# Kernel tuning notes

Measured on AMD Instinct MI355X. Metric: run time of the kernel, lower is better.

The kernel has to match this reference:

```python
import jax, jax.numpy as jnp
import numpy as np
from jax import lax

BN_EPS = 1e-5


def setup_inputs() -> dict:
    key = jax.random.key(0)
    ks = jax.random.split(key, 12)
    h, c, i, kk = 8, 64, 96, 3
    c2, n, d = c // 2, 8, 512
    std = lambda f: np.float32(f)
    return {
        "X": jax.random.normal(ks[0], (h, n, d), jnp.float32),
        "lin_w": jax.random.normal(ks[1], (h, c2, d), jnp.float32) * std(d ** -0.5),
        "lin_b": jax.random.normal(ks[2], (h, c2), jnp.float32) * std(0.02),
        "bn_gamma": jnp.ones((h, c2), jnp.float32),
        "bn_beta": jnp.zeros((h, c2), jnp.float32),
        "px": jax.random.normal(ks[3], (1, 1, c2, 1, i), jnp.float32) * std(c ** -0.5),
        "py": jax.random.normal(ks[4], (1, 1, c2, i, 1), jnp.float32) * std(c ** -0.5),
        "kw": jax.random.normal(ks[5], (h, c, c), jnp.float32) * std(c ** -0.5),
        "kb": jax.random.normal(ks[6], (h, c), jnp.float32) * std(0.02),
        "vw": jax.random.normal(ks[7], (h, c, c), jnp.float32) * std(c ** -0.5),
        "vb": jax.random.normal(ks[8], (h, c), jnp.float32) * std(0.02),
        "sw": jax.random.normal(ks[9], (c, c, kk, kk), jnp.float32) * std((c * kk * kk) ** -0.5),
        "sb": jax.random.normal(ks[10], (c,), jnp.float32) * std(0.02),
    }


def reference(X, lin_w, lin_b, bn_gamma, bn_beta, px, py, kw, kb, vw, vb, sw, sb):
    h, n, _ = X.shape
    c = kw.shape[1]
    c2 = c // 2
    i = px.shape[-1]
    kk = sw.shape[-1]

    # --- MultiheadEmbedding: per-head Linear -> BatchNorm1d(train) -> ReLU ---
    y = jnp.einsum('hnd,hcd->hnc', X, lin_w) + lin_b[:, None, :]      # (h, n, c2)
    mu = y.mean(axis=1, keepdims=True)
    var = y.var(axis=1, keepdims=True)                                 # biased, as BN
    y = (y - mu) * lax.rsqrt(var + BN_EPS) * bn_gamma[:, None, :] + bn_beta[:, None, :]
    y = jax.nn.relu(y)
    M = jnp.transpose(y, (1, 0, 2))[..., None, None]                   # (n, h, c2, 1, 1)

    # --- PositionalEncoding: concat x/y translated copies -> (n, h, c, i, i) ---
    P = jnp.concatenate([
        jnp.broadcast_to(M + px, (n, h, c2, i, i)),
        jnp.broadcast_to(M + py, (n, h, c2, i, i)),
    ], axis=2)                                                          # (n, h, c, i, i)

    # --- TransposeAttention ---
    # grouped 1x1 key conv (groups = h)
    kp = jnp.einsum('nhcij,hdc->nhdij', P, kw) + kb[None, :, :, None, None]
    # score conv over each (c, i, i) map, shared across heads, scaled
    x = kp.reshape(n * h, c, i, i)
    s = lax.conv_general_dilated(x, sw, (1, 1), 'SAME',
                                 dimension_numbers=('NCHW', 'OIHW', 'NCHW'))
    s = (s + sb[None, :, None, None]) / np.float32((c * kk * kk) ** 0.5)
    w = jax.nn.softmax(s.reshape(n, h, c, i, i), axis=1)                # softmax over heads
    # grouped 1x1 value conv, weighted sum over heads
    vp = jnp.einsum('nhcij,hdc->nhdij', P, vw) + vb[None, :, :, None, None]
    T = (w * vp).sum(axis=1)                                            # (n, c, i, i)
    return (T, M, P, w)
```

## Files before the change

kernel.cpp:

```cpp
#include <hip/hip_runtime.h>
#include <math.h>

#define H    8
#define N    8
#define D    512
#define C    64
#define C2   32
#define I    96
#define II   9216

#define OFF_T 0
#define OFF_M 4718592
#define OFF_P 4720640
#define OFF_W 42469376

#define WS_AK 0
#define WS_AV 4096
#define WS_BK 8192
#define WS_BV 57344
#define WS_CK 106496
#define WS_CV 155648
#define WS_SS 204800
#define WS_SP 241664
#define WS_SQ 278528
#define WS_F  315392
#define WS_G2 352256
#define WS_H2 499712

__device__ __forceinline__ int bcls(int x) { return x == 0 ? 0 : (x == I - 1 ? 2 : 1); }

__global__ __launch_bounds__(256) void irf_embed(
    const float* __restrict__ X, const float* __restrict__ lin_w,
    const float* __restrict__ lin_b, const float* __restrict__ gamma,
    const float* __restrict__ beta, float* __restrict__ out)
{
    const int h = blockIdx.x, t = threadIdx.x;
    const int n = t >> 5, cc = t & 31;

    __shared__ float Xs[N * D];
    __shared__ float ys[N * C2];
    __shared__ float scale_s[C2], shift_s[C2];

    const float4* Xg  = (const float4*)(X + (size_t)h * N * D);
    float4*       Xs4 = (float4*)Xs;
    for (int idx = t; idx < N * D / 4; idx += 256) Xs4[idx] = Xg[idx];
    __syncthreads();

    const float4* wrow = (const float4*)(lin_w + ((size_t)h * C2 + cc) * D);
    const float4* xrow = (const float4*)(Xs + n * D);
    float a0 = 0.f, a1 = 0.f, a2 = 0.f, a3 = 0.f;
    #pragma unroll 4
    for (int k = 0; k < D / 4; ++k) {
        float4 xv = xrow[k], wv = wrow[k];
        a0 = fmaf(xv.x, wv.x, a0); a1 = fmaf(xv.y, wv.y, a1);
        a2 = fmaf(xv.z, wv.z, a2); a3 = fmaf(xv.w, wv.w, a3);
    }
    float y = (a0 + a1) + (a2 + a3) + lin_b[h * C2 + cc];
    ys[n * C2 + cc] = y;
    __syncthreads();

    if (t < C2) {
        float s = 0.f, ss = 0.f;
        #pragma unroll
        for (int j = 0; j < N; ++j) { float v = ys[j * C2 + t]; s += v; ss += v * v; }
        float mu  = s * (1.0f / N);
        float var = ss * (1.0f / N) - mu * mu;
        float sc  = rsqrtf(var + 1e-5f) * gamma[h * C2 + t];
        scale_s[t] = sc;
        shift_s[t] = beta[h * C2 + t] - mu * sc;
    }
    __syncthreads();

    float v = fmaxf(fmaf(y, scale_s[cc], shift_s[cc]), 0.0f);
    out[OFF_M + (n * H + h) * C2 + cc] = v;
}

__global__ __launch_bounds__(256) void irf_factors_a(
    const float* __restrict__ kw, const float* __restrict__ kb,
    const float* __restrict__ vw, const float* __restrict__ vb,
    const float* __restrict__ px, const float* __restrict__ py,
    const float* __restrict__ sw, const float* __restrict__ out,
    float* __restrict__ ws)
{
    int gid = blockIdx.x * 256 + threadIdx.x;
    if (gid < 4096) {
        int id = gid, d = id & 63, h = (id >> 6) & 7, n = id >> 9;
        const float* kwr = kw + ((size_t)h * C + d) * C;
        const float* vwr = vw + ((size_t)h * C + d) * C;
        const float* Mr  = out + OFF_M + (n * H + h) * C2;
        float ak = kb[h * C + d], av = vb[h * C + d];
        #pragma unroll 8
        for (int c = 0; c < C2; ++c) {
            float m = Mr[c];
            ak = fmaf(kwr[c] + kwr[C2 + c], m, ak);
            av = fmaf(vwr[c] + vwr[C2 + c], m, av);
        }
        ws[WS_AK + id] = ak;
        ws[WS_AV + id] = av;
    } else if (gid < 4096 + 49152) {
        int id = gid - 4096, d = id & 63, r = id >> 6, b = r % I, h = r / I;
        const float* kwr = kw + ((size_t)h * C + d) * C;
        const float* vwr = vw + ((size_t)h * C + d) * C;
        float bk = 0.f, bv = 0.f, ck = 0.f, cv = 0.f;
        #pragma unroll 8
        for (int c = 0; c < C2; ++c) {
            float pxv = px[c * I + b], pyv = py[c * I + b];
            bk = fmaf(kwr[c], pxv, bk);       bv = fmaf(vwr[c], pxv, bv);
            ck = fmaf(kwr[C2 + c], pyv, ck);  cv = fmaf(vwr[C2 + c], pyv, cv);
        }
        ws[WS_BK + id] = bk;
        ws[WS_BV + (h * C + d) * I + b] = bv;
        ws[WS_CK + id] = ck; ws[WS_CV + id] = cv;
    } else if (gid < 4096 + 49152 + 4096) {
        int id = gid - (4096 + 49152), d = id & 63, e = id >> 6;
        float k9[3][3];
        const float* swr = sw + (size_t)(e * C + d) * 9;
        #pragma unroll
        for (int p = 0; p < 3; ++p)
            #pragma unroll
            for (int q = 0; q < 3; ++q) k9[p][q] = swr[p * 3 + q];
        #pragma unroll
        for (int ra = 0; ra < 3; ++ra) {
            int pmin = (ra == 0) ? 1 : 0, pmax = (ra == 2) ? 1 : 2;
            #pragma unroll
            for (int q = 0; q < 3; ++q) {
                float sp = 0.f;
                for (int p = pmin; p <= pmax; ++p) sp += k9[p][q];
                ws[WS_SP + ((ra * 3 + q) * C + e) * C + d] = sp;
            }
            #pragma unroll
            for (int rb = 0; rb < 3; ++rb) {
                int qmin = (rb == 0) ? 1 : 0, qmax = (rb == 2) ? 1 : 2;
                float ssv = 0.f;
                for (int p = pmin; p <= pmax; ++p)
                    for (int q = qmin; q <= qmax; ++q) ssv += k9[p][q];
                ws[WS_SS + ((ra * 3 + rb) * C + e) * C + d] = ssv;
            }
        }
        #pragma unroll
        for (int rb = 0; rb < 3; ++rb) {
            int qmin = (rb == 0) ? 1 : 0, qmax = (rb == 2) ? 1 : 2;
            #pragma unroll
            for (int p = 0; p < 3; ++p) {
                float sq = 0.f;
                for (int q = qmin; q <= qmax; ++q) sq += k9[p][q];
                ws[WS_SQ + ((rb * 3 + p) * C + e) * C + d] = sq;
            }
        }
    }
}

__global__ __launch_bounds__(256) void irf_factors_b(float* __restrict__ ws)
{
    int gid = blockIdx.x * 256 + threadIdx.x;
    if (gid < 36864) {
        int id = gid, e = id & 63, h = (id >> 6) & 7, cls = (id >> 9) % 9, n = id / 4608;
        const float* ak = ws + WS_AK + (n * H + h) * C;
        const float* ss = ws + WS_SS + (cls * C + e) * C;
        float acc = 0.f;
        #pragma unroll 8
        for (int d = 0; d < C; ++d) acc = fmaf(ak[d], ss[d], acc);
        ws[WS_F + id] = acc;
    } else if (gid < 36864 + 147456) {
        int j = gid - 36864, b = j % I, e = (j / I) & 63, h = (j / (I * C)) & 7, ra = j / (I * C * H);
        int rb = bcls(b), qmin = (rb == 0) ? 1 : 0, qmax = (rb == 2) ? 1 : 2;
        float acc = 0.f;
        for (int q = qmin; q <= qmax; ++q) {
            const float* sp = ws + WS_SP + ((ra * 3 + q) * C + e) * C;
            const float* bk = ws + WS_BK + ((h * I) + (b + q - 1)) * C;
            #pragma unroll 8
            for (int d = 0; d < C; ++d) acc = fmaf(sp[d], bk[d], acc);
        }
        ws[WS_G2 + j] = acc;
    } else if (gid < 36864 + 2 * 147456) {
        int j = gid - 36864 - 147456, e = j & 63, h = (j >> 6) & 7, rb = (j >> 9) % 3, a = j / 1536;
        int ra = bcls(a), pmin = (ra == 0) ? 1 : 0, pmax = (ra == 2) ? 1 : 2;
        float acc = 0.f;
        for (int p = pmin; p <= pmax; ++p) {
            const float* sq = ws + WS_SQ + ((rb * 3 + p) * C + e) * C;
            const float* ck = ws + WS_CK + ((h * I) + (a + p - 1)) * C;
            #pragma unroll 8
            for (int d = 0; d < C; ++d) acc = fmaf(sq[d], ck[d], acc);
        }
        ws[WS_H2 + j] = acc;
    }
}

__global__ __launch_bounds__(256) void irf_site(
    const float* __restrict__ px, const float* __restrict__ py,
    const float* __restrict__ sb, const float* __restrict__ ws,
    float* __restrict__ out)
{
    const int bid = blockIdx.x;
    const int n = bid / I, a = bid - n * I;
    const int ra = bcls(a);
    const int t = threadIdx.x;

    __shared__ float FH[3 * 512];
    __shared__ float AC[512];
    __shared__ float Ms_[256];
    __shared__ float pxs[C2 * I];
    __shared__ float pys[C2];

    {
        const float* fsrc = ws + WS_F + (n * 9 + ra * 3) * 512;
        const float* hsrc = ws + WS_H2 + a * 1536;
        for (int o = t; o < 1536; o += 256) FH[o] = fsrc[o] + hsrc[o] + sb[o & 63];
        const float* avsrc = ws + WS_AV + n * 512;
        for (int o = t; o < 512; o += 256) {
            int h = o >> 6, e = o & 63;
            AC[o] = avsrc[o] + ws[WS_CV + ((h * I) + a) * C + e];
        }
        Ms_[t] = out[OFF_M + n * 256 + t];
        for (int o = t; o < C2 * I; o += 256) pxs[o] = px[o];
        if (t < C2) pys[t] = py[t * I + a];
    }
    __syncthreads();

    const float inv24 = 1.0f / 24.0f;

    #pragma unroll
    for (int it = 0; it < 6; ++it) {
        int idx = it * 256 + t;
        int e = idx / 24, b4 = idx - e * 24;
        int b = b4 * 4;

        float4 sv[H];
        float4 mx = make_float4(-1e30f, -1e30f, -1e30f, -1e30f);
        #pragma unroll
        for (int h = 0; h < H; ++h) {
            float4 g2 = ((const float4*)(ws + WS_G2 + ((ra * H + h) * C + e) * I))[b4];
            float fh1 = FH[512 + h * 64 + e];
            float fx = fh1, fw = fh1;
            if (b4 == 0)  fx = FH[h * 64 + e];
            if (b4 == 23) fw = FH[1024 + h * 64 + e];
            float4 s;
            s.x = (fx  + g2.x) * inv24;
            s.y = (fh1 + g2.y) * inv24;
            s.z = (fh1 + g2.z) * inv24;
            s.w = (fw  + g2.w) * inv24;
            sv[h] = s;
            mx.x = fmaxf(mx.x, s.x); mx.y = fmaxf(mx.y, s.y);
            mx.z = fmaxf(mx.z, s.z); mx.w = fmaxf(mx.w, s.w);
        }
        float4 sum = make_float4(0.f, 0.f, 0.f, 0.f);
        #pragma unroll
        for (int h = 0; h < H; ++h) {
            sv[h].x = __expf(sv[h].x - mx.x); sum.x += sv[h].x;
            sv[h].y = __expf(sv[h].y - mx.y); sum.y += sv[h].y;
            sv[h].z = __expf(sv[h].z - mx.z); sum.z += sv[h].z;
            sv[h].w = __expf(sv[h].w - mx.w); sum.w += sv[h].w;
        }
        float4 rs;
        rs.x = 1.0f / sum.x; rs.y = 1.0f / sum.y;
        rs.z = 1.0f / sum.z; rs.w = 1.0f / sum.w;

        float4 T = make_float4(0.f, 0.f, 0.f, 0.f);
        #pragma unroll
        for (int h = 0; h < H; ++h) {
            float4 w;
            w.x = sv[h].x * rs.x; w.y = sv[h].y * rs.y;
            w.z = sv[h].z * rs.z; w.w = sv[h].w * rs.w;
            ((float4*)(out + OFF_W + (size_t)(((n * H + h) * C + e) * I + a) * I))[b4] = w;
            float ac = AC[h * 64 + e];
            float4 bv = ((const float4*)(ws + WS_BV + (h * C + e) * I))[b4];
            T.x = fmaf(w.x, ac + bv.x, T.x);
            T.y = fmaf(w.y, ac + bv.y, T.y);
            T.z = fmaf(w.z, ac + bv.z, T.z);
            T.w = fmaf(w.w, ac + bv.w, T.w);
        }
        ((float4*)(out + OFF_T + (size_t)((n * C + e) * I + a) * I))[b4] = T;
    }

    #pragma unroll
    for (int it = 0; it < 48; ++it) {
        int idx = it * 256 + t;
        int b4 = idx % 24, rem = idx / 24;
        int c = rem & 63, h = rem >> 6;
        float4 v;
        if (c < C2) {
            float base = Ms_[h * C2 + c];
            float4 p4 = ((const float4*)(pxs + c * I))[b4];
            v.x = base + p4.x; v.y = base + p4.y;
            v.z = base + p4.z; v.w = base + p4.w;
        } else {
            float bb = Ms_[h * C2 + c - C2] + pys[c - C2];
            v = make_float4(bb, bb, bb, bb);
        }
        ((float4*)(out + OFF_P + (size_t)(((n * H + h) * C + c) * I + a) * I))[b4] = v;
    }
}

extern "C" void kernel_launch(void* const* d_in, const int* in_sizes, int n_in,
                              void* d_out, int out_size, void* d_ws, size_t ws_size,
                              hipStream_t stream) {
    const float* X     = (const float*)d_in[0];
    const float* lin_w = (const float*)d_in[1];
    const float* lin_b = (const float*)d_in[2];
    const float* gamma = (const float*)d_in[3];
    const float* beta  = (const float*)d_in[4];
    const float* px    = (const float*)d_in[5];
    const float* py    = (const float*)d_in[6];
    const float* kw    = (const float*)d_in[7];
    const float* kb    = (const float*)d_in[8];
    const float* vw    = (const float*)d_in[9];
    const float* vb    = (const float*)d_in[10];
    const float* sw    = (const float*)d_in[11];
    const float* sb    = (const float*)d_in[12];

    float* out = (float*)d_out;
    float* ws  = (float*)d_ws;

    irf_embed    <<<8,    256, 0, stream>>>(X, lin_w, lin_b, gamma, beta, out);
    irf_factors_a<<<224,  256, 0, stream>>>(kw, kb, vw, vb, px, py, sw, out, ws);
    irf_factors_b<<<1296, 256, 0, stream>>>(ws);
    irf_site     <<<768,  256, 0, stream>>>(px, py, sb, ws, out);
}
```

Before: 411.6 us.

## Restructure site kernel into per-plane softmax and P-write kernels with transposed factors

Splits the per-(n,a) site kernel into a softmax kernel organized per (n,e) plane and a separate P-write kernel per (n,h,c) plane, so output stores become fully contiguous plane writes. Factor tables are stored transposed and padded (zero halo columns) so the G2/H2 convolution factors are computed with float4 sliding-window FMAs, producing four outputs per thread. The aim is coalesced writes and fewer redundant loads. The cost is an extra kernel launch and the extra padding-zeroing work in the factor kernel.

After: 392.9 us. 1.05x faster.

```diff
diff --git a/kernel.cpp b/kernel.cpp
--- a/kernel.cpp
+++ b/kernel.cpp
@@ -14,18 +14,18 @@
 #define OFF_P 4720640
 #define OFF_W 42469376
 
-#define WS_AK 0
-#define WS_AV 4096
-#define WS_BK 8192
-#define WS_BV 57344
-#define WS_CK 106496
-#define WS_CV 155648
-#define WS_SS 204800
-#define WS_SP 241664
-#define WS_SQ 278528
-#define WS_F  315392
-#define WS_G2 352256
-#define WS_H2 499712
+#define WS_AK    0
+#define WS_AV    4096
+#define WS_BV    8192
+#define WS_CVT   57344
+#define WS_BKT2  106496
+#define WS_CKT2  157696
+#define WS_SST   208896
+#define WS_SPT   245760
+#define WS_SQT   282624
+#define WS_F     319488
+#define WS_G2    356352
+#define WS_H2    503808
 
 __device__ __forceinline__ int bcls(int x) { return x == 0 ? 0 : (x == I - 1 ? 2 : 1); }
 
@@ -108,9 +108,10 @@
             bk = fmaf(kwr[c], pxv, bk);       bv = fmaf(vwr[c], pxv, bv);
             ck = fmaf(kwr[C2 + c], pyv, ck);  cv = fmaf(vwr[C2 + c], pyv, cv);
         }
-        ws[WS_BK + id] = bk;
-        ws[WS_BV + (h * C + d) * I + b] = bv;
-        ws[WS_CK + id] = ck; ws[WS_CV + id] = cv;
+        ws[WS_BKT2 + (h * C + d) * 100 + (b + 1)] = bk;
+        ws[WS_BV   + (h * C + d) * I   + b]       = bv;
+        ws[WS_CKT2 + (h * C + d) * 100 + (b + 1)] = ck;
+        ws[WS_CVT  + (h * C + d) * I   + b]       = cv;
     } else if (gid < 4096 + 49152 + 4096) {
         int id = gid - (4096 + 49152), d = id & 63, e = id >> 6;
         float k9[3][3];
@@ -126,7 +127,7 @@
             for (int q = 0; q < 3; ++q) {
                 float sp = 0.f;
                 for (int p = pmin; p <= pmax; ++p) sp += k9[p][q];
-                ws[WS_SP + ((ra * 3 + q) * C + e) * C + d] = sp;
+                ws[WS_SPT + ((ra * 3 + q) * C + d) * C + e] = sp;
             }
             #pragma unroll
             for (int rb = 0; rb < 3; ++rb) {
@@ -134,7 +135,7 @@
                 float ssv = 0.f;
                 for (int p = pmin; p <= pmax; ++p)
                     for (int q = qmin; q <= qmax; ++q) ssv += k9[p][q];
-                ws[WS_SS + ((ra * 3 + rb) * C + e) * C + d] = ssv;
+                ws[WS_SST + ((ra * 3 + rb) * C + d) * C + e] = ssv;
             }
         }
         #pragma unroll
@@ -144,9 +145,15 @@
             for (int p = 0; p < 3; ++p) {
                 float sq = 0.f;
                 for (int q = qmin; q <= qmax; ++q) sq += k9[p][q];
-                ws[WS_SQ + ((rb * 3 + p) * C + e) * C + d] = sq;
+                ws[WS_SQT + ((rb * 3 + p) * C + d) * C + e] = sq;
             }
         }
+    } else {
+        int s = gid - (4096 + 49152 + 4096);
+        int d = s & 63, h = (s >> 6) & 7, k = s >> 9;
+        int col = (k & 3) == 0 ? 0 : 96 + (k & 3);
+        int base = (k >> 2) ? WS_CKT2 : WS_BKT2;
+        ws[base + (h * C + d) * 100 + col] = 0.f;
     }
 }
 
@@ -154,91 +161,103 @@
 {
     int gid = blockIdx.x * 256 + threadIdx.x;
     if (gid < 36864) {
-        int id = gid, e = id & 63, h = (id >> 6) & 7, cls = (id >> 9) % 9, n = id / 4608;
-        const float* ak = ws + WS_AK + (n * H + h) * C;
-        const float* ss = ws + WS_SS + (cls * C + e) * C;
+        int e = gid & 63, h = (gid >> 6) & 7, cls = (gid >> 9) % 9, n = gid / 4608;
+        const float* ak  = ws + WS_AK + (n * H + h) * C;
+        const float* sst = ws + WS_SST + cls * (C * C) + e;
         float acc = 0.f;
         #pragma unroll 8
-        for (int d = 0; d < C; ++d) acc = fmaf(ak[d], ss[d], acc);
-        ws[WS_F + id] = acc;
-    } else if (gid < 36864 + 147456) {
-        int j = gid - 36864, b = j % I, e = (j / I) & 63, h = (j / (I * C)) & 7, ra = j / (I * C * H);
-        int rb = bcls(b), qmin = (rb == 0) ? 1 : 0, qmax = (rb == 2) ? 1 : 2;
-        float acc = 0.f;
-        for (int q = qmin; q <= qmax; ++q) {
-            const float* sp = ws + WS_SP + ((ra * 3 + q) * C + e) * C;
-            const float* bk = ws + WS_BK + ((h * I) + (b + q - 1)) * C;
-            #pragma unroll 8
-            for (int d = 0; d < C; ++d) acc = fmaf(sp[d], bk[d], acc);
-        }
-        ws[WS_G2 + j] = acc;
-    } else if (gid < 36864 + 2 * 147456) {
-        int j = gid - 36864 - 147456, e = j & 63, h = (j >> 6) & 7, rb = (j >> 9) % 3, a = j / 1536;
-        int ra = bcls(a), pmin = (ra == 0) ? 1 : 0, pmax = (ra == 2) ? 1 : 2;
-        float acc = 0.f;
-        for (int p = pmin; p <= pmax; ++p) {
-            const float* sq = ws + WS_SQ + ((rb * 3 + p) * C + e) * C;
-            const float* ck = ws + WS_CK + ((h * I) + (a + p - 1)) * C;
-            #pragma unroll 8
-            for (int d = 0; d < C; ++d) acc = fmaf(sq[d], ck[d], acc);
-        }
-        ws[WS_H2 + j] = acc;
-    }
-}
-
-__global__ __launch_bounds__(256) void irf_site(
-    const float* __restrict__ px, const float* __restrict__ py,
+        for (int d = 0; d < C; ++d) acc = fmaf(ak[d], sst[d * C], acc);
+        ws[WS_F + gid] = acc;
+    } else if (gid < 73728) {
+        int j = gid - 36864;
+        int b4 = j % 24, e = (j / 24) & 63, h = (j / 1536) & 7, ra = j / 12288;
+        const float* sp  = ws + WS_SPT + (ra * 3) * (C * C) + e;
+        const float* row = ws + WS_BKT2 + h * (C * 100) + 4 * b4;
+        float4 acc = make_float4(0.f, 0.f, 0.f, 0.f);
+        #pragma unroll 4
+        for (int d = 0; d < C; ++d) {
+            float s0 = sp[d * C], s1 = sp[4096 + d * C], s2 = sp[8192 + d * C];
+            float4 A = *(const float4*)(row + d * 100);
+            float4 B = *(const float4*)(row + d * 100 + 4);
+            acc.x = fmaf(s0, A.x, fmaf(s1, A.y, fmaf(s2, A.z, acc.x)));
+            acc.y = fmaf(s0, A.y, fmaf(s1, A.z, fmaf(s2, A.w, acc.y)));
+            acc.z = fmaf(s0, A.z, fmaf(s1, A.w, fmaf(s2, B.x, acc.z)));
+            acc.w = fmaf(s0, A.w, fmaf(s1, B.x, fmaf(s2, B.y, acc.w)));
+        }
+        ((float4*)(ws + WS_G2 + ((ra * H + h) * C + e) * I))[b4] = acc;
+    } else {
+        int j = gid - 73728;
+        int a4 = j % 24, e = (j / 24) & 63, h = (j / 1536) & 7, rb = j / 12288;
+        const float* sq  = ws + WS_SQT + (rb * 3) * (C * C) + e;
+        const float* row = ws + WS_CKT2 + h * (C * 100) + 4 * a4;
+        float4 acc = make_float4(0.f, 0.f, 0.f, 0.f);
+        #pragma unroll 4
+        for (int d = 0; d < C; ++d) {
+            float s0 = sq[d * C], s1 = sq[4096 + d * C], s2 = sq[8192 + d * C];
+            float4 A = *(const float4*)(row + d * 100);
+            float4 B = *(const float4*)(row + d * 100 + 4);
+            acc.x = fmaf(s0, A.x, fmaf(s1, A.y, fmaf(s2, A.z, acc.x)));
+            acc.y = fmaf(s0, A.y, fmaf(s1, A.z, fmaf(s2, A.w, acc.y)));
+            acc.z = fmaf(s0, A.z, fmaf(s1, A.w, fmaf(s2, B.x, acc.z)));
+            acc.w = fmaf(s0, A.w, fmaf(s1, B.x, fmaf(s2, B.y, acc.w)));
+        }
+        ((float4*)(ws + WS_H2 + ((rb * H + h) * C + e) * I))[a4] = acc;
+    }
+}
+
+__global__ __launch_bounds__(256) void irf_softmax(
     const float* __restrict__ sb, const float* __restrict__ ws,
     float* __restrict__ out)
 {
     const int bid = blockIdx.x;
-    const int n = bid / I, a = bid - n * I;
-    const int ra = bcls(a);
+    const int n = bid >> 6, e = bid & 63;
     const int t = threadIdx.x;
 
-    __shared__ float FH[3 * 512];
-    __shared__ float AC[512];
-    __shared__ float Ms_[256];
-    __shared__ float pxs[C2 * I];
-    __shared__ float pys[C2];
-
-    {
-        const float* fsrc = ws + WS_F + (n * 9 + ra * 3) * 512;
-        const float* hsrc = ws + WS_H2 + a * 1536;
-        for (int o = t; o < 1536; o += 256) FH[o] = fsrc[o] + hsrc[o] + sb[o & 63];
-        const float* avsrc = ws + WS_AV + n * 512;
-        for (int o = t; o < 512; o += 256) {
-            int h = o >> 6, e = o & 63;
-            AC[o] = avsrc[o] + ws[WS_CV + ((h * I) + a) * C + e];
-        }
-        Ms_[t] = out[OFF_M + n * 256 + t];
-        for (int o = t; o < C2 * I; o += 256) pxs[o] = px[o];
-        if (t < C2) pys[t] = py[t * I + a];
-    }
+    __shared__ __align__(16) float G2s[3 * H * I];
+    __shared__ __align__(16) float H2s[3 * H * I];
+    __shared__ __align__(16) float BVs[H * I];
+    __shared__ float CVs[H * I];
+    __shared__ float Fs[9 * H];
+    __shared__ float AVs[H];
+
+    for (int o = t; o < 3 * H * I; o += 256) {
+        int rh = o / I, sp = o - rh * I;
+        G2s[o] = ws[WS_G2 + (rh * C + e) * I + sp];
+        H2s[o] = ws[WS_H2 + (rh * C + e) * I + sp];
+    }
+    for (int o = t; o < H * I; o += 256) {
+        int h = o / I, sp = o - h * I;
+        BVs[o] = ws[WS_BV  + (h * C + e) * I + sp];
+        CVs[o] = ws[WS_CVT + (h * C + e) * I + sp];
+    }
+    if (t < 9 * H) Fs[t] = ws[WS_F + ((n * 9 + t / 8) * H + (t & 7)) * C + e];
+    if (t < H)     AVs[t] = ws[WS_AV + (n * H + t) * C + e];
+    const float sbv = sb[e];
     __syncthreads();
 
     const float inv24 = 1.0f / 24.0f;
+    float4* Tplane = (float4*)(out + OFF_T + (size_t)(n * C + e) * II);
 
     #pragma unroll
-    for (int it = 0; it < 6; ++it) {
+    for (int it = 0; it < 9; ++it) {
         int idx = it * 256 + t;
-        int e = idx / 24, b4 = idx - e * 24;
-        int b = b4 * 4;
+        int a = idx / 24, b4 = idx - a * 24;
+        int ra = bcls(a);
 
         float4 sv[H];
         float4 mx = make_float4(-1e30f, -1e30f, -1e30f, -1e30f);
         #pragma unroll
         for (int h = 0; h < H; ++h) {
-            float4 g2 = ((const float4*)(ws + WS_G2 + ((ra * H + h) * C + e) * I))[b4];
-            float fh1 = FH[512 + h * 64 + e];
-            float fx = fh1, fw = fh1;
-            if (b4 == 0)  fx = FH[h * 64 + e];
-            if (b4 == 23) fw = FH[1024 + h * 64 + e];
+            float4 g2 = ((const float4*)(G2s + (ra * H + h) * I))[b4];
+            float f1 = Fs[(ra * 3 + 1) * H + h] + H2s[(H + h) * I + a] + sbv;
+            float fx = f1, fw = f1;
+            if (b4 == 0)  fx = Fs[(ra * 3 + 0) * H + h] + H2s[h * I + a] + sbv;
+            if (b4 == 23) fw = Fs[(ra * 3 + 2) * H + h] + H2s[(2 * H + h) * I + a] + sbv;
             float4 s;
-            s.x = (fx  + g2.x) * inv24;
-            s.y = (fh1 + g2.y) * inv24;
-            s.z = (fh1 + g2.z) * inv24;
-            s.w = (fw  + g2.w) * inv24;
+            s.x = (fx + g2.x) * inv24;
+            s.y = (f1 + g2.y) * inv24;
+            s.z = (f1 + g2.z) * inv24;
+            s.w = (fw + g2.w) * inv24;
             sv[h] = s;
             mx.x = fmaxf(mx.x, s.x); mx.y = fmaxf(mx.y, s.y);
             mx.z = fmaxf(mx.z, s.z); mx.w = fmaxf(mx.w, s.w);
@@ -261,33 +280,50 @@
             float4 w;
             w.x = sv[h].x * rs.x; w.y = sv[h].y * rs.y;
             w.z = sv[h].z * rs.z; w.w = sv[h].w * rs.w;
-            ((float4*)(out + OFF_W + (size_t)(((n * H + h) * C + e) * I + a) * I))[b4] = w;
-            float ac = AC[h * 64 + e];
-            float4 bv = ((const float4*)(ws + WS_BV + (h * C + e) * I))[b4];
+            ((float4*)(out + OFF_W + (size_t)((n * H + h) * C + e) * II))[idx] = w;
+            float ac = AVs[h] + CVs[h * I + a];
+            float4 bv = ((const float4*)(BVs + h * I))[b4];
             T.x = fmaf(w.x, ac + bv.x, T.x);
             T.y = fmaf(w.y, ac + bv.y, T.y);
             T.z = fmaf(w.z, ac + bv.z, T.z);
             T.w = fmaf(w.w, ac + bv.w, T.w);
         }
-        ((float4*)(out + OFF_T + (size_t)((n * C + e) * I + a) * I))[b4] = T;
-    }
-
-    #pragma unroll
-    for (int it = 0; it < 48; ++it) {
-        int idx = it * 256 + t;
-        int b4 = idx % 24, rem = idx / 24;
-        int c = rem & 63, h = rem >> 6;
-        float4 v;
-        if (c < C2) {
-            float base = Ms_[h * C2 + c];
-            float4 p4 = ((const float4*)(pxs + c * I))[b4];
-            v.x = base + p4.x; v.y = base + p4.y;
-            v.z = base + p4.z; v.w = base + p4.w;
-        } else {
-            float bb = Ms_[h * C2 + c - C2] + pys[c - C2];
-            v = make_float4(bb, bb, bb, bb);
-        }
-        ((float4*)(out + OFF_P + (size_t)(((n * H + h) * C + c) * I + a) * I))[b4] = v;
+        Tplane[idx] = T;
+    }
+}
+
+__global__ __launch_bounds__(256) void irf_pwrite(
+    const float* __restrict__ px, const float* __restrict__ py,
+    float* __restrict__ out)
+{
+    const int bid = blockIdx.x;
+    const int c = bid & 63, nh = bid >> 6;
+    const int t = threadIdx.x;
+
+    __shared__ __align__(16) float rowp[I];
+    const float m = out[OFF_M + nh * C2 + (c & 31)];
+    if (t < I / 4) {
+        const float* src = (c < C2) ? (px + c * I) : (py + (c - C2) * I);
+        ((float4*)rowp)[t] = ((const float4*)src)[t];
+    }
+    __syncthreads();
+
+    float4* plane = (float4*)(out + OFF_P + (size_t)bid * II);
+    if (c < C2) {
+        #pragma unroll
+        for (int it = 0; it < 9; ++it) {
+            int idx = it * 256 + t;
+            float4 v = ((const float4*)rowp)[idx % 24];
+            v.x += m; v.y += m; v.z += m; v.w += m;
+            plane[idx] = v;
+        }
+    } else {
+        #pragma unroll
+        for (int it = 0; it < 9; ++it) {
+            int idx = it * 256 + t;
+            float vv = m + rowp[idx / 24];
+            plane[idx] = make_float4(vv, vv, vv, vv);
+        }
     }
 }
 
@@ -312,7 +348,8 @@
     float* ws  = (float*)d_ws;
 
     irf_embed    <<<8,    256, 0, stream>>>(X, lin_w, lin_b, gamma, beta, out);
-    irf_factors_a<<<224,  256, 0, stream>>>(kw, kb, vw, vb, px, py, sw, out, ws);
-    irf_factors_b<<<1296, 256, 0, stream>>>(ws);
-    irf_site     <<<768,  256, 0, stream>>>(px, py, sb, ws, out);
-}
+    irf_factors_a<<<240,  256, 0, stream>>>(kw, kb, vw, vb, px, py, sw, out, ws);
+    irf_factors_b<<<432,  256, 0, stream>>>(ws);
+    irf_softmax  <<<512,  256, 0, stream>>>(sb, ws, out);
+    irf_pwrite   <<<4096, 256, 0, stream>>>(px, py, out);
+}
```
